# Performance work log

Hardware: AMD Instinct MI355X
Metric: run time of the kernel (lower is better)

## Reference

```python
import jax, jax.numpy as jnp
import numpy as np

DIM = 1024
NUM_HEADS = 16
HEAD_DIM = 64
SEQ_LEN = 4096
RMS_EPS = 1e-6


def rotary_tables(T, head_dim):
    # modded-nanogpt style rotary: frequencies only on first half of the half-dim,
    # second half zeroed (identity rotation).
    angular_freq = (1.0 / 1024.0) ** jnp.linspace(0.0, 1.0, head_dim // 4)
    angular_freq = jnp.concatenate([angular_freq, jnp.zeros(head_dim // 4)])
    t = jnp.arange(T, dtype=jnp.float32)
    theta = t[:, None] * angular_freq[None, :]  # [T, D/2]
    return jnp.cos(theta), jnp.sin(theta)


def apply_rotary(x, cos, sin):
    # x: [B, T, H, D]
    xf = x.astype(jnp.float32)
    x1, x2 = jnp.split(xf, 2, axis=-1)
    c = cos[None, :, None, :]
    s = sin[None, :, None, :]
    y1 = x1 * c + x2 * s
    y2 = x1 * (-s) + x2 * c
    return jnp.concatenate([y1, y2], axis=-1).astype(x.dtype)


def rms_norm(x):
    return x * jax.lax.rsqrt(jnp.mean(x * x, axis=-1, keepdims=True) + RMS_EPS)


def setup_inputs() -> dict:
    key = jax.random.key(0)
    k1, k2, k3 = jax.random.split(key, 3)
    hdim = NUM_HEADS * HEAD_DIM
    std = 0.5 * DIM ** (-0.5)
    bound = (3.0 ** 0.5) * std
    x = jax.random.normal(k1, (1, SEQ_LEN, DIM), dtype=jnp.float32)
    qkv_w = jax.random.uniform(k2, (3 * hdim, DIM), minval=-bound, maxval=bound, dtype=jnp.float32)
    # original zero-inits c_proj; use small random weights for a nontrivial baseline
    proj_w = jax.random.normal(k3, (DIM, hdim), dtype=jnp.float32) * 0.02
    lambdas = jnp.array([0.5], dtype=jnp.float32)
    return {"x": x, "qkv_w": qkv_w, "lambdas": lambdas, "proj_w": proj_w}


def reference(x, qkv_w, lambdas, proj_w):
    B, T, _ = x.shape
    H, D = NUM_HEADS, HEAD_DIM
    scale = 1.0 / (D ** 0.5)
    qkv = jnp.einsum('btc,fc->btf', x, qkv_w)            # [B, T, 3*H*D]
    qkv = qkv.reshape(B, T, 3 * H, D)
    q, k, v = jnp.split(qkv, 3, axis=-2)                  # each [B, T, H, D]
    q, k = rms_norm(q), rms_norm(k)
    cos, sin = rotary_tables(T, D)
    q, k = apply_rotary(q, cos, sin), apply_rotary(k, cos, sin)
    v = lambdas[0] * v
    scores = jnp.einsum('bqhd,bkhd->bhqk', q, k) * scale  # [B, H, T, T]
    causal = jnp.tril(jnp.ones((T, T), dtype=bool))
    scores = jnp.where(causal[None, None], scores, -jnp.inf)
    p = jax.nn.softmax(scores, axis=-1)
    y = jnp.einsum('bhqk,bkhd->bqhd', p, v)               # [B, T, H, D]
    y = y.reshape(B, T, H * D)
    return jnp.einsum('btf,cf->btc', y, proj_w)           # [B, T, DIM]
```

## Files before the change

kernel.cpp:

```cpp
#include <hip/hip_runtime.h>
#include <stdint.h>

#define SEQ 4096
#define NHEAD 16
#define HDIM 64

typedef __attribute__((ext_vector_type(4))) float f32x4;
typedef __attribute__((ext_vector_type(16))) float f32x16;
typedef __attribute__((ext_vector_type(8))) __bf16 bf16x8;
typedef __attribute__((ext_vector_type(8))) unsigned short u16x8;
typedef __attribute__((ext_vector_type(4))) unsigned short u16x4;
typedef __attribute__((ext_vector_type(4))) unsigned int u32x4;

static __device__ __forceinline__ float bf2f(unsigned short u) {
    unsigned int x = ((unsigned int)u) << 16;
    return __builtin_bit_cast(float, x);
}
static __device__ __forceinline__ unsigned short f2bf(float f) {
    unsigned int u = __builtin_bit_cast(unsigned int, f);
    u += 0x7FFFu + ((u >> 16) & 1u);
    return (unsigned short)(u >> 16);
}
static __device__ __forceinline__ f32x4 mfma_bf16_16x16x32(u16x8 a, u16x8 b, f32x4 c) {
    return __builtin_amdgcn_mfma_f32_16x16x32_bf16(
        __builtin_bit_cast(bf16x8, a), __builtin_bit_cast(bf16x8, b), c, 0, 0, 0);
}
static __device__ __forceinline__ f32x16 mfma_bf16_32x32x16(u16x8 a, u16x8 b, f32x16 c) {
    return __builtin_amdgcn_mfma_f32_32x32x16_bf16(
        __builtin_bit_cast(bf16x8, a), __builtin_bit_cast(bf16x8, b), c, 0, 0, 0);
}
static __device__ __forceinline__ void gload_lds16(const void* g, void* l) {
    __builtin_amdgcn_global_load_lds(
        (__attribute__((address_space(1))) unsigned int*)g,
        (__attribute__((address_space(3))) unsigned int*)l,
        16, 0, 0);
}
static __device__ __forceinline__ unsigned int cvtpk_bf16(float lo, float hi) {
    unsigned int r;
    asm("v_cvt_pk_bf16_f32 %0, %1, %2" : "=v"(r) : "v"(lo), "v"(hi));
    return r;
}

__global__ void cvt3_kernel(const float* __restrict__ s0, unsigned short* __restrict__ d0, int n0q,
                            const float* __restrict__ s1, unsigned short* __restrict__ d1, int n1q,
                            const float* __restrict__ s2, unsigned short* __restrict__ d2, int n2q)
{
    const int stride = gridDim.x * blockDim.x;
    const int total = n0q + n1q + n2q;
    for (int i = blockIdx.x * blockDim.x + threadIdx.x; i < total; i += stride) {
        const float* src; unsigned short* dst; int j;
        if (i < n0q)            { src = s0; dst = d0; j = i; }
        else if (i < n0q + n1q) { src = s1; dst = d1; j = i - n0q; }
        else                    { src = s2; dst = d2; j = i - n0q - n1q; }
        f32x4 v = *(const f32x4*)(src + (size_t)j * 4);
        u16x4 o;
#pragma unroll
        for (int k = 0; k < 4; k++) o[k] = f2bf(v[k]);
        *(u16x4*)(dst + (size_t)j * 4) = o;
    }
}

template<int OUT_BF16, int BN>
__global__ __launch_bounds__(256) void gemm_bt_kernel(
    const unsigned short* __restrict__ A,
    const unsigned short* __restrict__ B,
    void* __restrict__ Cv,
    int M, int N, int K, int lda)
{
    constexpr int NJ = BN / 32;
    __shared__ __align__(16) unsigned short As[128 * 64];
    __shared__ __align__(16) unsigned short Bs[BN * 64];
    const int tid = threadIdx.x;
    const int lane = tid & 63;
    const int wave = tid >> 6;
    const int wm = (wave >> 1) * 64;
    const int wn = (wave & 1) * (BN / 2);
    const int bm = blockIdx.y * 128, bn = blockIdx.x * BN;
    const int l15 = lane & 15, l4 = lane >> 4;

    f32x4 acc[4][NJ];
#pragma unroll
    for (int i = 0; i < 4; i++)
#pragma unroll
        for (int j = 0; j < NJ; j++) acc[i][j] = (f32x4){0.f, 0.f, 0.f, 0.f};

    const int srow = tid >> 3;
    const int scol = (tid & 7) * 8;
    const unsigned short* Ab = A + (size_t)(bm + srow) * lda + scol;
    const unsigned short* Bb = B + (size_t)(bn + srow) * K + scol;

    for (int kt = 0; kt < K; kt += 64) {
#pragma unroll
        for (int ci = 0; ci < 4; ci++)
            gload_lds16(Ab + (size_t)ci * 32 * lda + kt, &As[ci * 2048 + tid * 8]);
#pragma unroll
        for (int ci = 0; ci < NJ; ci++)
            gload_lds16(Bb + (size_t)ci * 32 * K + kt, &Bs[ci * 2048 + tid * 8]);
        __syncthreads();
#pragma unroll
        for (int ks = 0; ks < 2; ks++) {
            const int kc = ks * 32 + l4 * 8;
            u16x8 af[4], bfr[NJ];
#pragma unroll
            for (int i = 0; i < 4; i++)
                af[i] = *(const u16x8*)&As[(wm + i * 16 + l15) * 64 + kc];
#pragma unroll
            for (int j = 0; j < NJ; j++)
                bfr[j] = *(const u16x8*)&Bs[(wn + j * 16 + l15) * 64 + kc];
#pragma unroll
            for (int i = 0; i < 4; i++)
#pragma unroll
                for (int j = 0; j < NJ; j++)
                    acc[i][j] = mfma_bf16_16x16x32(af[i], bfr[j], acc[i][j]);
        }
        __syncthreads();
    }

    const int orow = bm + wm + l4 * 4;
    const int ocol = bn + wn + l15;
#pragma unroll
    for (int i = 0; i < 4; i++)
#pragma unroll
        for (int j = 0; j < NJ; j++)
#pragma unroll
            for (int r = 0; r < 4; r++) {
                size_t idx = (size_t)(orow + i * 16 + r) * N + (ocol + j * 16);
                if (OUT_BF16) ((unsigned short*)Cv)[idx] = f2bf(acc[i][j][r]);
                else          ((float*)Cv)[idx] = acc[i][j][r];
            }
}

__global__ __launch_bounds__(256) void rope_norm_kernel(
    const unsigned short* __restrict__ qkv,
    const float* __restrict__ lambdas,
    unsigned short* __restrict__ qh,
    unsigned short* __restrict__ kh,
    unsigned short* __restrict__ vh)
{
    const int lane = threadIdx.x & 63;
    const int wave = threadIdx.x >> 6;
    const int vec = blockIdx.x * 4 + wave;
    const int t = vec >> 4;
    const int h = vec & 15;
    const size_t base = (size_t)t * 3072 + h * 64 + lane;
    float q = bf2f(qkv[base]);
    float k = bf2f(qkv[base + 1024]);
    float v = bf2f(qkv[base + 2048]);
    float sq = q * q, sk = k * k;
#pragma unroll
    for (int m = 1; m < 64; m <<= 1) {
        sq += __shfl_xor(sq, m);
        sk += __shfl_xor(sk, m);
    }
    q *= rsqrtf(sq * (1.0f / 64.0f) + 1e-6f);
    k *= rsqrtf(sk * (1.0f / 64.0f) + 1e-6f);
    const int i = lane & 31;
    float w = (i < 16) ? exp2f(-(10.0f / 15.0f) * (float)i) : 0.0f;
    float th = (float)t * w;
    float c = cosf(th), s = sinf(th);
    float qp = __shfl_xor(q, 32);
    float kp = __shfl_xor(k, 32);
    float sg = (lane < 32) ? s : -s;
    float qo = (q * c + qp * sg) * 0.1803368801111244f;
    float ko = k * c + kp * sg;
    float vo = v * lambdas[0];
    const size_t o = ((size_t)h * SEQ + t) * 64 + lane;
    qh[o] = f2bf(qo);
    kh[o] = f2bf(ko);
    vh[o] = f2bf(vo);
}

__global__ __launch_bounds__(256) void transpose_v_kernel(
    const unsigned short* __restrict__ vh, unsigned short* __restrict__ vT)
{
    __shared__ __align__(16) unsigned short tile[64][72];
    const int h = blockIdx.x >> 6;
    const int tt = (blockIdx.x & 63) * 64;
    const int tid = threadIdx.x;
    const int row = tid >> 2;
    const int c0 = (tid & 3) * 16;
    const u16x8* src = (const u16x8*)(vh + ((size_t)h * SEQ + tt + row) * 64 + c0);
    u16x8 a = src[0], b = src[1];
#pragma unroll
    for (int j = 0; j < 8; j++) { tile[row][c0 + j] = a[j]; tile[row][c0 + 8 + j] = b[j]; }
    __syncthreads();
    u16x8 o0, o1;
#pragma unroll
    for (int j = 0; j < 8; j++) { o0[j] = tile[c0 + j][row]; o1[j] = tile[c0 + 8 + j][row]; }
    u16x8* dst = (u16x8*)(vT + ((size_t)h * 64 + row) * SEQ + tt + c0);
    dst[0] = o0; dst[1] = o1;
}

__global__ __launch_bounds__(256, 3) void attn_kernel(
    const unsigned short* __restrict__ qh,
    const unsigned short* __restrict__ kh,
    const unsigned short* __restrict__ vT,
    float* __restrict__ acc,
    float* __restrict__ lacc)
{
    __shared__ __align__(16) unsigned short Ks[2][64 * 64];
    __shared__ __align__(16) unsigned short Vs[2][64 * 64];
    const int h = blockIdx.x;
    const int qp = blockIdx.y;
    const int s = blockIdx.z;
    const int tid = threadIdx.x;
    const int lane = tid & 63;
    const int wave = tid >> 6;
    const int l31 = lane & 31;
    const int hi = lane >> 5;
    const int r7 = l31 & 7;

    const unsigned short* Kb = kh + (size_t)h * SEQ * 64;
    const unsigned short* Vb = vT + (size_t)h * 64 * SEQ;

    const int sr = tid >> 3;
    const int scs = ((tid & 7) * 8) ^ ((sr & 7) * 8);

#pragma unroll 1
    for (int ph = 0; ph < 2; ph++) {
        const int qtp = ph ? (31 - qp) : qp;
        const int nt = 2 * qtp + 2;
        const int t0 = (nt * s) / 3;
        const int t1 = (nt * (s + 1)) / 3;
        if (t0 >= t1) continue;
        const int q0w = qtp * 128 + wave * 32;

        u16x8 qf[4];
        {
            const unsigned short* qb = qh + ((size_t)h * SEQ + q0w + l31) * 64 + hi * 8;
#pragma unroll
            for (int c = 0; c < 4; c++) qf[c] = *(const u16x8*)(qb + c * 16);
        }

        f32x16 o0 = {}, o1 = {};
        float l = 0.f;

        const unsigned short* kst = Kb + (size_t)(t0 * 64 + sr) * 64 + scs;
        const unsigned short* vst = Vb + (size_t)sr * SEQ + t0 * 64 + scs;

        gload_lds16(kst,            &Ks[0][tid * 8]);
        gload_lds16(kst + 32 * 64,  &Ks[0][2048 + tid * 8]);
        gload_lds16(vst,            &Vs[0][tid * 8]);
        gload_lds16(vst + 32 * SEQ, &Vs[0][2048 + tid * 8]);
        kst += 64 * 64;
        vst += 64;
        __syncthreads();

        int cur = 0;
        for (int kt = t0; kt < t1; kt++) {
            const int kv0 = kt * 64;
            if (kt + 1 < t1) {
                gload_lds16(kst,            &Ks[cur ^ 1][tid * 8]);
                gload_lds16(kst + 32 * 64,  &Ks[cur ^ 1][2048 + tid * 8]);
                gload_lds16(vst,            &Vs[cur ^ 1][tid * 8]);
                gload_lds16(vst + 32 * SEQ, &Vs[cur ^ 1][2048 + tid * 8]);
            }
            kst += 64 * 64;
            vst += 64;
            if (kv0 <= q0w + 31) {
                const unsigned short* ks0 = &Ks[cur][l31 * 64];
                const unsigned short* vs0 = &Vs[cur][l31 * 64];
                const unsigned short* ks1 = ks0 + 32 * 64;
                const unsigned short* vs1 = vs0 + 32 * 64;
                const bool half2 = (kv0 + 32 <= q0w + 31);
                const int q = q0w + l31;
                float ts;

                {
                    f32x16 st = {};
                    __builtin_amdgcn_s_setprio(1);
#pragma unroll
                    for (int c = 0; c < 4; c++) {
                        const int off = ((c * 2 + hi) ^ r7) * 8;
                        st = mfma_bf16_32x32x16(*(const u16x8*)(ks0 + off), qf[c], st);
                    }
                    __builtin_amdgcn_s_setprio(0);
                    if (kv0 + 31 > q0w) {
#pragma unroll
                        for (int r = 0; r < 16; r++) {
                            const int crow = (r & 3) + 8 * (r >> 2) + 4 * hi;
                            if (kv0 + crow > q) st[r] = -1e30f;
                        }
                    }
#pragma unroll
                    for (int r = 0; r < 16; r++) st[r] = exp2f(st[r]);
                    float u8[8];
#pragma unroll
                    for (int r = 0; r < 8; r++) u8[r] = st[r] + st[r + 8];
#pragma unroll
                    for (int r = 0; r < 4; r++) u8[r] += u8[r + 4];
                    ts = (u8[0] + u8[2]) + (u8[1] + u8[3]);

                    u16x8 paf[2];
#pragma unroll
                    for (int kk = 0; kk < 2; kk++) {
                        const int rb = kk * 8;
                        unsigned int a0 = cvtpk_bf16(st[rb + 0], st[rb + 1]);
                        unsigned int a1 = cvtpk_bf16(st[rb + 2], st[rb + 3]);
                        unsigned int b0 = cvtpk_bf16(st[rb + 4], st[rb + 5]);
                        unsigned int b1 = cvtpk_bf16(st[rb + 6], st[rb + 7]);
                        asm("v_permlane32_swap_b32 %0, %1" : "+v"(a0), "+v"(b0));
                        asm("v_permlane32_swap_b32 %0, %1" : "+v"(a1), "+v"(b1));
                        u32x4 w;
                        w[0] = a0; w[1] = a1; w[2] = b0; w[3] = b1;
                        paf[kk] = __builtin_bit_cast(u16x8, w);
                    }
                    __builtin_amdgcn_s_setprio(1);
#pragma unroll
                    for (int kk = 0; kk < 2; kk++) {
                        const int off = ((kk * 2 + hi) ^ r7) * 8;
                        u16x8 v0 = *(const u16x8*)(vs0 + off);
                        u16x8 v1 = *(const u16x8*)(vs1 + off);
                        o0 = mfma_bf16_32x32x16(paf[kk], v0, o0);
                        o1 = mfma_bf16_32x32x16(paf[kk], v1, o1);
                    }
                    __builtin_amdgcn_s_setprio(0);
                }

                if (half2) {
                    f32x16 st = {};
                    __builtin_amdgcn_s_setprio(1);
#pragma unroll
                    for (int c = 0; c < 4; c++) {
                        const int off = ((c * 2 + hi) ^ r7) * 8;
                        st = mfma_bf16_32x32x16(*(const u16x8*)(ks1 + off), qf[c], st);
                    }
                    __builtin_amdgcn_s_setprio(0);
                    if (kv0 + 63 > q0w) {
#pragma unroll
                        for (int r = 0; r < 16; r++) {
                            const int crow = (r & 3) + 8 * (r >> 2) + 4 * hi;
                            if (kv0 + 32 + crow > q) st[r] = -1e30f;
                        }
                    }
#pragma unroll
                    for (int r = 0; r < 16; r++) st[r] = exp2f(st[r]);
                    float u8[8];
#pragma unroll
                    for (int r = 0; r < 8; r++) u8[r] = st[r] + st[r + 8];
#pragma unroll
                    for (int r = 0; r < 4; r++) u8[r] += u8[r + 4];
                    ts += (u8[0] + u8[2]) + (u8[1] + u8[3]);

                    u16x8 paf[2];
#pragma unroll
                    for (int kk = 0; kk < 2; kk++) {
                        const int rb = kk * 8;
                        unsigned int a0 = cvtpk_bf16(st[rb + 0], st[rb + 1]);
                        unsigned int a1 = cvtpk_bf16(st[rb + 2], st[rb + 3]);
                        unsigned int b0 = cvtpk_bf16(st[rb + 4], st[rb + 5]);
                        unsigned int b1 = cvtpk_bf16(st[rb + 6], st[rb + 7]);
                        asm("v_permlane32_swap_b32 %0, %1" : "+v"(a0), "+v"(b0));
                        asm("v_permlane32_swap_b32 %0, %1" : "+v"(a1), "+v"(b1));
                        u32x4 w;
                        w[0] = a0; w[1] = a1; w[2] = b0; w[3] = b1;
                        paf[kk] = __builtin_bit_cast(u16x8, w);
                    }
                    __builtin_amdgcn_s_setprio(1);
#pragma unroll
                    for (int kk = 0; kk < 2; kk++) {
                        const int off = (((kk + 2) * 2 + hi) ^ r7) * 8;
                        u16x8 v0 = *(const u16x8*)(vs0 + off);
                        u16x8 v1 = *(const u16x8*)(vs1 + off);
                        o0 = mfma_bf16_32x32x16(paf[kk], v0, o0);
                        o1 = mfma_bf16_32x32x16(paf[kk], v1, o1);
                    }
                    __builtin_amdgcn_s_setprio(0);
                }

                ts += __shfl_xor(ts, 32);
                l += ts;
            }
            __syncthreads();
            cur ^= 1;
        }

        if (t0 * 64 <= q0w + 31) {
#pragma unroll
            for (int r = 0; r < 16; r++) {
                const int crow = (r & 3) + 8 * (r >> 2) + 4 * hi;
                float* row = acc + (size_t)(q0w + crow) * 1024 + h * 64;
                atomicAdd(row + l31,      o0[r]);
                atomicAdd(row + 32 + l31, o1[r]);
            }
            if (hi == 0) atomicAdd(lacc + (size_t)(q0w + l31) * 16 + h, l);
        }
    }
}

__global__ __launch_bounds__(256) void norm_kernel(
    const float* __restrict__ acc, const float* __restrict__ lacc,
    unsigned short* __restrict__ yb)
{
    const int i = blockIdx.x * 256 + threadIdx.x;
    const int t = i >> 8;
    const int h = (i & 255) >> 4;
    const float inv = 1.0f / lacc[t * 16 + h];
    f32x4 v = *(const f32x4*)(acc + (size_t)i * 4);
    u16x4 o;
#pragma unroll
    for (int j = 0; j < 4; j++) o[j] = f2bf(v[j] * inv);
    *(u16x4*)(yb + (size_t)i * 4) = o;
}

extern "C" void kernel_launch(void* const* d_in, const int* in_sizes, int n_in,
                              void* d_out, int out_size, void* d_ws, size_t ws_size,
                              hipStream_t stream) {
    (void)in_sizes; (void)n_in; (void)out_size; (void)ws_size;
    const float* x       = (const float*)d_in[0];
    const float* qkv_w   = (const float*)d_in[1];
    const float* lambdas = (const float*)d_in[2];
    const float* proj_w  = (const float*)d_in[3];

    char* ws = (char*)d_ws;
    unsigned short* x_bf   = (unsigned short*)(ws + 0);
    unsigned short* qkv_bf = (unsigned short*)(ws + 8388608);
    unsigned short* qh     = (unsigned short*)(ws + 33554432);
    unsigned short* kh     = (unsigned short*)(ws + 41943040);
    unsigned short* vh     = (unsigned short*)(ws + 50331648);
    unsigned short* vT     = (unsigned short*)(ws + 58720256);
    unsigned short* wq_bf  = (unsigned short*)(ws + 67108864);
    unsigned short* wp_bf  = (unsigned short*)(ws + 73400320);
    unsigned short* yb     = (unsigned short*)(ws + 75497472);
    float*          acc    = (float*)(ws + 0);
    float*          lacc   = (float*)(ws + 16777216);

    cvt3_kernel<<<2048, 256, 0, stream>>>(x, x_bf, 1048576,
                                          qkv_w, wq_bf, 786432,
                                          proj_w, wp_bf, 262144);

    gemm_bt_kernel<1, 64><<<dim3(48, 32), 256, 0, stream>>>(x_bf, wq_bf, qkv_bf, 4096, 3072, 1024, 1024);
    rope_norm_kernel<<<16384, 256, 0, stream>>>(qkv_bf, lambdas, qh, kh, vh);
    transpose_v_kernel<<<1024, 256, 0, stream>>>(vh, vT);

    hipMemsetAsync(ws, 0, 16777216 + 262144, stream);

    attn_kernel<<<dim3(16, 16, 3), 256, 0, stream>>>(qh, kh, vT, acc, lacc);
    norm_kernel<<<4096, 256, 0, stream>>>(acc, lacc, yb);

    gemm_bt_kernel<0, 64><<<dim3(16, 32), 256, 0, stream>>>(yb, wp_bf, d_out, 4096, 1024, 1024, 1024);
}
```

Measured before the change: 180.4 us.

## Fuse RMS norm, rotary and V transpose into QKV GEMM epilogue

Result: no change. 182.2 us (+1.0%).

```diff
diff --git a/kernel.cpp b/kernel.cpp
--- a/kernel.cpp
+++ b/kernel.cpp
@@ -60,16 +60,20 @@
     }
 }
 
-template<int OUT_BF16, int BN>
+template<int MODE, int BN>
 __global__ __launch_bounds__(256) void gemm_bt_kernel(
     const unsigned short* __restrict__ A,
     const unsigned short* __restrict__ B,
     void* __restrict__ Cv,
+    unsigned short* __restrict__ khp,
+    unsigned short* __restrict__ vTp,
+    const float* __restrict__ lambdas,
     int M, int N, int K, int lda)
 {
     constexpr int NJ = BN / 32;
-    __shared__ __align__(16) unsigned short As[128 * 64];
-    __shared__ __align__(16) unsigned short Bs[BN * 64];
+    __shared__ __align__(16) unsigned short smem[128 * 64 + BN * 64];
+    unsigned short* As = smem;
+    unsigned short* Bs = smem + 128 * 64;
     const int tid = threadIdx.x;
     const int lane = tid & 63;
     const int wave = tid >> 6;
@@ -116,79 +120,70 @@
         __syncthreads();
     }
 
-    const int orow = bm + wm + l4 * 4;
-    const int ocol = bn + wn + l15;
-#pragma unroll
-    for (int i = 0; i < 4; i++)
-#pragma unroll
-        for (int j = 0; j < NJ; j++)
-#pragma unroll
-            for (int r = 0; r < 4; r++) {
-                size_t idx = (size_t)(orow + i * 16 + r) * N + (ocol + j * 16);
-                if (OUT_BF16) ((unsigned short*)Cv)[idx] = f2bf(acc[i][j][r]);
-                else          ((float*)Cv)[idx] = acc[i][j][r];
+    if constexpr (MODE == 0) {
+        const int orow = bm + wm + l4 * 4;
+        const int ocol = bn + wn + l15;
+#pragma unroll
+        for (int i = 0; i < 4; i++)
+#pragma unroll
+            for (int j = 0; j < NJ; j++)
+#pragma unroll
+                for (int r = 0; r < 4; r++) {
+                    size_t idx = (size_t)(orow + i * 16 + r) * N + (ocol + j * 16);
+                    ((float*)Cv)[idx] = acc[i][j][r];
+                }
+    } else {
+        unsigned short* tile = smem;
+        const int type = bn >> 10;
+        const int h = (bn & 1023) >> 6;
+#pragma unroll
+        for (int i = 0; i < 4; i++)
+#pragma unroll
+            for (int j = 0; j < NJ; j++)
+#pragma unroll
+                for (int r = 0; r < 4; r++)
+                    tile[(wm + i * 16 + l4 * 4 + r) * 66 + wn + j * 16 + l15] =
+                        f2bf(acc[i][j][r]);
+        __syncthreads();
+
+        if (type == 2) {
+            const float lam = lambdas[0];
+            const int drow = tid >> 2;
+            const int c0 = (tid & 3) * 16;
+#pragma unroll
+            for (int p = 0; p < 2; p++) {
+                u16x8 o0, o1;
+#pragma unroll
+                for (int j = 0; j < 8; j++) {
+                    o0[j] = f2bf(bf2f(tile[(p * 64 + c0 + j) * 66 + drow]) * lam);
+                    o1[j] = f2bf(bf2f(tile[(p * 64 + c0 + 8 + j) * 66 + drow]) * lam);
+                }
+                u16x8* dst = (u16x8*)(vTp + ((size_t)h * 64 + drow) * SEQ + bm + p * 64 + c0);
+                dst[0] = o0; dst[1] = o1;
             }
-}
-
-__global__ __launch_bounds__(256) void rope_norm_kernel(
-    const unsigned short* __restrict__ qkv,
-    const float* __restrict__ lambdas,
-    unsigned short* __restrict__ qh,
-    unsigned short* __restrict__ kh,
-    unsigned short* __restrict__ vh)
-{
-    const int lane = threadIdx.x & 63;
-    const int wave = threadIdx.x >> 6;
-    const int vec = blockIdx.x * 4 + wave;
-    const int t = vec >> 4;
-    const int h = vec & 15;
-    const size_t base = (size_t)t * 3072 + h * 64 + lane;
-    float q = bf2f(qkv[base]);
-    float k = bf2f(qkv[base + 1024]);
-    float v = bf2f(qkv[base + 2048]);
-    float sq = q * q, sk = k * k;
-#pragma unroll
-    for (int m = 1; m < 64; m <<= 1) {
-        sq += __shfl_xor(sq, m);
-        sk += __shfl_xor(sk, m);
+        } else {
+            unsigned short* outp = (type == 0) ? (unsigned short*)Cv : khp;
+            const int i31 = lane & 31;
+            const float wfreq = (i31 < 16) ? exp2f(-(10.0f / 15.0f) * (float)i31) : 0.0f;
+            const float qscale = (type == 0) ? 0.1803368801111244f : 1.0f;
+#pragma unroll 1
+            for (int it = 0; it < 32; it++) {
+                const int tl = it * 4 + wave;
+                const int t = bm + tl;
+                float v = bf2f(tile[tl * 66 + lane]);
+                float sq = v * v;
+#pragma unroll
+                for (int m = 1; m < 64; m <<= 1) sq += __shfl_xor(sq, m);
+                v *= rsqrtf(sq * (1.0f / 64.0f) + 1e-6f);
+                const float th = (float)t * wfreq;
+                const float c = cosf(th), s = sinf(th);
+                const float vp = __shfl_xor(v, 32);
+                const float sg = (lane < 32) ? s : -s;
+                const float out = (v * c + vp * sg) * qscale;
+                outp[((size_t)h * SEQ + t) * 64 + lane] = f2bf(out);
+            }
+        }
     }
-    q *= rsqrtf(sq * (1.0f / 64.0f) + 1e-6f);
-    k *= rsqrtf(sk * (1.0f / 64.0f) + 1e-6f);
-    const int i = lane & 31;
-    float w = (i < 16) ? exp2f(-(10.0f / 15.0f) * (float)i) : 0.0f;
-    float th = (float)t * w;
-    float c = cosf(th), s = sinf(th);
-    float qp = __shfl_xor(q, 32);
-    float kp = __shfl_xor(k, 32);
-    float sg = (lane < 32) ? s : -s;
-    float qo = (q * c + qp * sg) * 0.1803368801111244f;
-    float ko = k * c + kp * sg;
-    float vo = v * lambdas[0];
-    const size_t o = ((size_t)h * SEQ + t) * 64 + lane;
-    qh[o] = f2bf(qo);
-    kh[o] = f2bf(ko);
-    vh[o] = f2bf(vo);
-}
-
-__global__ __launch_bounds__(256) void transpose_v_kernel(
-    const unsigned short* __restrict__ vh, unsigned short* __restrict__ vT)
-{
-    __shared__ __align__(16) unsigned short tile[64][72];
-    const int h = blockIdx.x >> 6;
-    const int tt = (blockIdx.x & 63) * 64;
-    const int tid = threadIdx.x;
-    const int row = tid >> 2;
-    const int c0 = (tid & 3) * 16;
-    const u16x8* src = (const u16x8*)(vh + ((size_t)h * SEQ + tt + row) * 64 + c0);
-    u16x8 a = src[0], b = src[1];
-#pragma unroll
-    for (int j = 0; j < 8; j++) { tile[row][c0 + j] = a[j]; tile[row][c0 + 8 + j] = b[j]; }
-    __syncthreads();
-    u16x8 o0, o1;
-#pragma unroll
-    for (int j = 0; j < 8; j++) { o0[j] = tile[c0 + j][row]; o1[j] = tile[c0 + 8 + j][row]; }
-    u16x8* dst = (u16x8*)(vT + ((size_t)h * 64 + row) * SEQ + tt + c0);
-    dst[0] = o0; dst[1] = o1;
 }
 
 __global__ __launch_bounds__(256, 3) void attn_kernel(
@@ -414,10 +409,8 @@
 
     char* ws = (char*)d_ws;
     unsigned short* x_bf   = (unsigned short*)(ws + 0);
-    unsigned short* qkv_bf = (unsigned short*)(ws + 8388608);
     unsigned short* qh     = (unsigned short*)(ws + 33554432);
     unsigned short* kh     = (unsigned short*)(ws + 41943040);
-    unsigned short* vh     = (unsigned short*)(ws + 50331648);
     unsigned short* vT     = (unsigned short*)(ws + 58720256);
     unsigned short* wq_bf  = (unsigned short*)(ws + 67108864);
     unsigned short* wp_bf  = (unsigned short*)(ws + 73400320);
@@ -429,14 +422,14 @@
                                           qkv_w, wq_bf, 786432,
                                           proj_w, wp_bf, 262144);
 
-    gemm_bt_kernel<1, 64><<<dim3(48, 32), 256, 0, stream>>>(x_bf, wq_bf, qkv_bf, 4096, 3072, 1024, 1024);
-    rope_norm_kernel<<<16384, 256, 0, stream>>>(qkv_bf, lambdas, qh, kh, vh);
-    transpose_v_kernel<<<1024, 256, 0, stream>>>(vh, vT);
+    gemm_bt_kernel<2, 64><<<dim3(48, 32), 256, 0, stream>>>(
+        x_bf, wq_bf, qh, kh, vT, lambdas, 4096, 3072, 1024, 1024);
 
     hipMemsetAsync(ws, 0, 16777216 + 262144, stream);
 
     attn_kernel<<<dim3(16, 16, 3), 256, 0, stream>>>(qh, kh, vT, acc, lacc);
     norm_kernel<<<4096, 256, 0, stream>>>(acc, lacc, yb);
 
-    gemm_bt_kernel<0, 64><<<dim3(16, 32), 256, 0, stream>>>(yb, wp_bf, d_out, 4096, 1024, 1024, 1024);
-}
+    gemm_bt_kernel<0, 64><<<dim3(16, 32), 256, 0, stream>>>(
+        yb, wp_bf, d_out, nullptr, nullptr, nullptr, 4096, 1024, 1024, 1024);
+}
```

## Process 64 query rows per wave to reuse K/V tiles across two Q blocks

Applied to the files above, without the earlier changes.

New measurement: 190.8 us. 1.06x slower.

```diff
diff --git a/kernel.cpp b/kernel.cpp
--- a/kernel.cpp
+++ b/kernel.cpp
@@ -191,7 +191,7 @@
     dst[0] = o0; dst[1] = o1;
 }
 
-__global__ __launch_bounds__(256, 3) void attn_kernel(
+__global__ __launch_bounds__(256, 2) void attn_kernel(
     const unsigned short* __restrict__ qh,
     const unsigned short* __restrict__ kh,
     const unsigned short* __restrict__ vT,
@@ -201,7 +201,7 @@
     __shared__ __align__(16) unsigned short Ks[2][64 * 64];
     __shared__ __align__(16) unsigned short Vs[2][64 * 64];
     const int h = blockIdx.x;
-    const int qp = blockIdx.y;
+    const int qpi = blockIdx.y;
     const int s = blockIdx.z;
     const int tid = threadIdx.x;
     const int lane = tid & 63;
@@ -218,22 +218,26 @@
 
 #pragma unroll 1
     for (int ph = 0; ph < 2; ph++) {
-        const int qtp = ph ? (31 - qp) : qp;
-        const int nt = 2 * qtp + 2;
-        const int t0 = (nt * s) / 3;
-        const int t1 = (nt * (s + 1)) / 3;
-        if (t0 >= t1) continue;
-        const int q0w = qtp * 128 + wave * 32;
-
-        u16x8 qf[4];
+        const int qtp = ph ? (15 - qpi) : qpi;
+        const int nt = 4 * (qtp + 1);
+        const int t0 = (qtp + 1) * s;
+        const int t1 = (qtp + 1) * (s + 1);
+        (void)nt;
+        const int q0w = qtp * 256 + wave * 64;
+
+        u16x8 qfA[4], qfB[4];
         {
-            const unsigned short* qb = qh + ((size_t)h * SEQ + q0w + l31) * 64 + hi * 8;
-#pragma unroll
-            for (int c = 0; c < 4; c++) qf[c] = *(const u16x8*)(qb + c * 16);
+            const unsigned short* qa = qh + ((size_t)h * SEQ + q0w + l31) * 64 + hi * 8;
+            const unsigned short* qb = qa + 32 * 64;
+#pragma unroll
+            for (int c = 0; c < 4; c++) {
+                qfA[c] = *(const u16x8*)(qa + c * 16);
+                qfB[c] = *(const u16x8*)(qb + c * 16);
+            }
         }
 
-        f32x16 o0 = {}, o1 = {};
-        float l = 0.f;
+        f32x16 oA0 = {}, oA1 = {}, oB0 = {}, oB1 = {};
+        float lA = 0.f, lB = 0.f;
 
         const unsigned short* kst = Kb + (size_t)(t0 * 64 + sr) * 64 + scs;
         const unsigned short* vst = Vb + (size_t)sr * SEQ + t0 * 64 + scs;
@@ -257,119 +261,116 @@
             }
             kst += 64 * 64;
             vst += 64;
-            if (kv0 <= q0w + 31) {
-                const unsigned short* ks0 = &Ks[cur][l31 * 64];
+            if (kv0 <= q0w + 63) {
                 const unsigned short* vs0 = &Vs[cur][l31 * 64];
-                const unsigned short* ks1 = ks0 + 32 * 64;
                 const unsigned short* vs1 = vs0 + 32 * 64;
-                const bool half2 = (kv0 + 32 <= q0w + 31);
-                const int q = q0w + l31;
-                float ts;
-
-                {
-                    f32x16 st = {};
-                    __builtin_amdgcn_s_setprio(1);
-#pragma unroll
-                    for (int c = 0; c < 4; c++) {
-                        const int off = ((c * 2 + hi) ^ r7) * 8;
-                        st = mfma_bf16_32x32x16(*(const u16x8*)(ks0 + off), qf[c], st);
-                    }
-                    __builtin_amdgcn_s_setprio(0);
-                    if (kv0 + 31 > q0w) {
-#pragma unroll
-                        for (int r = 0; r < 16; r++) {
-                            const int crow = (r & 3) + 8 * (r >> 2) + 4 * hi;
-                            if (kv0 + crow > q) st[r] = -1e30f;
+                float tsA = 0.f, tsB = 0.f;
+#pragma unroll
+                for (int hh = 0; hh < 2; hh++) {
+                    const int kvh = kv0 + 32 * hh;
+                    const bool doB = (kvh <= q0w + 63);
+                    if (!doB) continue;
+                    const bool doA = (kvh <= q0w + 31);
+                    const unsigned short* ksb = &Ks[cur][(32 * hh + l31) * 64];
+                    u16x8 kf[4];
+#pragma unroll
+                    for (int c = 0; c < 4; c++)
+                        kf[c] = *(const u16x8*)(ksb + (((c * 2 + hi) ^ r7) * 8));
+
+                    u16x8 pafA[2], pafB[2];
+                    if (doA) {
+                        f32x16 st = {};
+                        __builtin_amdgcn_s_setprio(1);
+#pragma unroll
+                        for (int c = 0; c < 4; c++)
+                            st = mfma_bf16_32x32x16(kf[c], qfA[c], st);
+                        __builtin_amdgcn_s_setprio(0);
+                        if (kvh + 31 > q0w) {
+                            const int q = q0w + l31;
+#pragma unroll
+                            for (int r = 0; r < 16; r++) {
+                                const int crow = (r & 3) + 8 * (r >> 2) + 4 * hi;
+                                if (kvh + crow > q) st[r] = -1e30f;
+                            }
+                        }
+#pragma unroll
+                        for (int r = 0; r < 16; r++) st[r] = exp2f(st[r]);
+                        float u8[8];
+#pragma unroll
+                        for (int r = 0; r < 8; r++) u8[r] = st[r] + st[r + 8];
+#pragma unroll
+                        for (int r = 0; r < 4; r++) u8[r] += u8[r + 4];
+                        tsA += (u8[0] + u8[2]) + (u8[1] + u8[3]);
+#pragma unroll
+                        for (int kk = 0; kk < 2; kk++) {
+                            const int rb = kk * 8;
+                            unsigned int a0 = cvtpk_bf16(st[rb + 0], st[rb + 1]);
+                            unsigned int a1 = cvtpk_bf16(st[rb + 2], st[rb + 3]);
+                            unsigned int b0 = cvtpk_bf16(st[rb + 4], st[rb + 5]);
+                            unsigned int b1 = cvtpk_bf16(st[rb + 6], st[rb + 7]);
+                            asm("v_permlane32_swap_b32 %0, %1" : "+v"(a0), "+v"(b0));
+                            asm("v_permlane32_swap_b32 %0, %1" : "+v"(a1), "+v"(b1));
+                            u32x4 w;
+                            w[0] = a0; w[1] = a1; w[2] = b0; w[3] = b1;
+                            pafA[kk] = __builtin_bit_cast(u16x8, w);
                         }
                     }
-#pragma unroll
-                    for (int r = 0; r < 16; r++) st[r] = exp2f(st[r]);
-                    float u8[8];
-#pragma unroll
-                    for (int r = 0; r < 8; r++) u8[r] = st[r] + st[r + 8];
-#pragma unroll
-                    for (int r = 0; r < 4; r++) u8[r] += u8[r + 4];
-                    ts = (u8[0] + u8[2]) + (u8[1] + u8[3]);
-
-                    u16x8 paf[2];
-#pragma unroll
-                    for (int kk = 0; kk < 2; kk++) {
-                        const int rb = kk * 8;
-                        unsigned int a0 = cvtpk_bf16(st[rb + 0], st[rb + 1]);
-                        unsigned int a1 = cvtpk_bf16(st[rb + 2], st[rb + 3]);
-                        unsigned int b0 = cvtpk_bf16(st[rb + 4], st[rb + 5]);
-                        unsigned int b1 = cvtpk_bf16(st[rb + 6], st[rb + 7]);
-                        asm("v_permlane32_swap_b32 %0, %1" : "+v"(a0), "+v"(b0));
-                        asm("v_permlane32_swap_b32 %0, %1" : "+v"(a1), "+v"(b1));
-                        u32x4 w;
-                        w[0] = a0; w[1] = a1; w[2] = b0; w[3] = b1;
-                        paf[kk] = __builtin_bit_cast(u16x8, w);
+                    {
+                        f32x16 st = {};
+                        __builtin_amdgcn_s_setprio(1);
+#pragma unroll
+                        for (int c = 0; c < 4; c++)
+                            st = mfma_bf16_32x32x16(kf[c], qfB[c], st);
+                        __builtin_amdgcn_s_setprio(0);
+                        if (kvh + 31 > q0w + 32) {
+                            const int q = q0w + 32 + l31;
+#pragma unroll
+                            for (int r = 0; r < 16; r++) {
+                                const int crow = (r & 3) + 8 * (r >> 2) + 4 * hi;
+                                if (kvh + crow > q) st[r] = -1e30f;
+                            }
+                        }
+#pragma unroll
+                        for (int r = 0; r < 16; r++) st[r] = exp2f(st[r]);
+                        float u8[8];
+#pragma unroll
+                        for (int r = 0; r < 8; r++) u8[r] = st[r] + st[r + 8];
+#pragma unroll
+                        for (int r = 0; r < 4; r++) u8[r] += u8[r + 4];
+                        tsB += (u8[0] + u8[2]) + (u8[1] + u8[3]);
+#pragma unroll
+                        for (int kk = 0; kk < 2; kk++) {
+                            const int rb = kk * 8;
+                            unsigned int a0 = cvtpk_bf16(st[rb + 0], st[rb + 1]);
+                            unsigned int a1 = cvtpk_bf16(st[rb + 2], st[rb + 3]);
+                            unsigned int b0 = cvtpk_bf16(st[rb + 4], st[rb + 5]);
+                            unsigned int b1 = cvtpk_bf16(st[rb + 6], st[rb + 7]);
+                            asm("v_permlane32_swap_b32 %0, %1" : "+v"(a0), "+v"(b0));
+                            asm("v_permlane32_swap_b32 %0, %1" : "+v"(a1), "+v"(b1));
+                            u32x4 w;
+                            w[0] = a0; w[1] = a1; w[2] = b0; w[3] = b1;
+                            pafB[kk] = __builtin_bit_cast(u16x8, w);
+                        }
                     }
                     __builtin_amdgcn_s_setprio(1);
 #pragma unroll
                     for (int kk = 0; kk < 2; kk++) {
-                        const int off = ((kk * 2 + hi) ^ r7) * 8;
+                        const int off = (((kk + 2 * hh) * 2 + hi) ^ r7) * 8;
                         u16x8 v0 = *(const u16x8*)(vs0 + off);
                         u16x8 v1 = *(const u16x8*)(vs1 + off);
-                        o0 = mfma_bf16_32x32x16(paf[kk], v0, o0);
-                        o1 = mfma_bf16_32x32x16(paf[kk], v1, o1);
+                        if (doA) {
+                            oA0 = mfma_bf16_32x32x16(pafA[kk], v0, oA0);
+                            oA1 = mfma_bf16_32x32x16(pafA[kk], v1, oA1);
+                        }
+                        oB0 = mfma_bf16_32x32x16(pafB[kk], v0, oB0);
+                        oB1 = mfma_bf16_32x32x16(pafB[kk], v1, oB1);
                     }
                     __builtin_amdgcn_s_setprio(0);
                 }
-
-                if (half2) {
-                    f32x16 st = {};
-                    __builtin_amdgcn_s_setprio(1);
-#pragma unroll
-                    for (int c = 0; c < 4; c++) {
-                        const int off = ((c * 2 + hi) ^ r7) * 8;
-                        st = mfma_bf16_32x32x16(*(const u16x8*)(ks1 + off), qf[c], st);
-                    }
-                    __builtin_amdgcn_s_setprio(0);
-                    if (kv0 + 63 > q0w) {
-#pragma unroll
-                        for (int r = 0; r < 16; r++) {
-                            const int crow = (r & 3) + 8 * (r >> 2) + 4 * hi;
-                            if (kv0 + 32 + crow > q) st[r] = -1e30f;
-                        }
-                    }
-#pragma unroll
-                    for (int r = 0; r < 16; r++) st[r] = exp2f(st[r]);
-                    float u8[8];
-#pragma unroll
-                    for (int r = 0; r < 8; r++) u8[r] = st[r] + st[r + 8];
-#pragma unroll
-                    for (int r = 0; r < 4; r++) u8[r] += u8[r + 4];
-                    ts += (u8[0] + u8[2]) + (u8[1] + u8[3]);
-
-                    u16x8 paf[2];
-#pragma unroll
-                    for (int kk = 0; kk < 2; kk++) {
-                        const int rb = kk * 8;
-                        unsigned int a0 = cvtpk_bf16(st[rb + 0], st[rb + 1]);
-                        unsigned int a1 = cvtpk_bf16(st[rb + 2], st[rb + 3]);
-                        unsigned int b0 = cvtpk_bf16(st[rb + 4], st[rb + 5]);
-                        unsigned int b1 = cvtpk_bf16(st[rb + 6], st[rb + 7]);
-                        asm("v_permlane32_swap_b32 %0, %1" : "+v"(a0), "+v"(b0));
-                        asm("v_permlane32_swap_b32 %0, %1" : "+v"(a1), "+v"(b1));
-                        u32x4 w;
-                        w[0] = a0; w[1] = a1; w[2] = b0; w[3] = b1;
-                        paf[kk] = __builtin_bit_cast(u16x8, w);
-                    }
-                    __builtin_amdgcn_s_setprio(1);
-#pragma unroll
-                    for (int kk = 0; kk < 2; kk++) {
-                        const int off = (((kk + 2) * 2 + hi) ^ r7) * 8;
-                        u16x8 v0 = *(const u16x8*)(vs0 + off);
-                        u16x8 v1 = *(const u16x8*)(vs1 + off);
-                        o0 = mfma_bf16_32x32x16(paf[kk], v0, o0);
-                        o1 = mfma_bf16_32x32x16(paf[kk], v1, o1);
-                    }
-                    __builtin_amdgcn_s_setprio(0);
-                }
-
-                ts += __shfl_xor(ts, 32);
-                l += ts;
+                tsA += __shfl_xor(tsA, 32);
+                tsB += __shfl_xor(tsB, 32);
+                lA += tsA;
+                lB += tsB;
             }
             __syncthreads();
             cur ^= 1;
@@ -380,10 +381,20 @@
             for (int r = 0; r < 16; r++) {
                 const int crow = (r & 3) + 8 * (r >> 2) + 4 * hi;
                 float* row = acc + (size_t)(q0w + crow) * 1024 + h * 64;
-                atomicAdd(row + l31,      o0[r]);
-                atomicAdd(row + 32 + l31, o1[r]);
-            }
-            if (hi == 0) atomicAdd(lacc + (size_t)(q0w + l31) * 16 + h, l);
+                atomicAdd(row + l31,      oA0[r]);
+                atomicAdd(row + 32 + l31, oA1[r]);
+            }
+            if (hi == 0) atomicAdd(lacc + (size_t)(q0w + l31) * 16 + h, lA);
+        }
+        if (t0 * 64 <= q0w + 63) {
+#pragma unroll
+            for (int r = 0; r < 16; r++) {
+                const int crow = (r & 3) + 8 * (r >> 2) + 4 * hi;
+                float* row = acc + (size_t)(q0w + 32 + crow) * 1024 + h * 64;
+                atomicAdd(row + l31,      oB0[r]);
+                atomicAdd(row + 32 + l31, oB1[r]);
+            }
+            if (hi == 0) atomicAdd(lacc + (size_t)(q0w + 32 + l31) * 16 + h, lB);
         }
     }
 }
@@ -435,7 +446,7 @@
 
     hipMemsetAsync(ws, 0, 16777216 + 262144, stream);
 
-    attn_kernel<<<dim3(16, 16, 3), 256, 0, stream>>>(qh, kh, vT, acc, lacc);
+    attn_kernel<<<dim3(16, 8, 4), 256, 0, stream>>>(qh, kh, vT, acc, lacc);
     norm_kernel<<<4096, 256, 0, stream>>>(acc, lacc, yb);
 
     gemm_bt_kernel<0, 64><<<dim3(16, 32), 256, 0, stream>>>(yb, wp_bf, d_out, 4096, 1024, 1024, 1024);
```
